# Optimization experiments

Measured on AMD Instinct MI355X. Metric: run time of the kernel, lower is better.

The kernel has to match this reference:

```python
import jax, jax.numpy as jnp
import numpy as np

N_CHARS = 256
EMB = 1024
HID = 2048
SEQ = 4096


def setup_inputs() -> dict:
    key = jax.random.key(0)
    ks = jax.random.split(key, 12)
    s = 0.02
    return {
        "input_seq": jax.random.randint(ks[0], (SEQ,), 0, N_CHARS),
        "hidden": jnp.zeros((HID,), jnp.float32),
        "cell": jnp.zeros((HID,), jnp.float32),
        "emb": jax.random.normal(ks[1], (N_CHARS, EMB), jnp.float32) * s,
        # gate weights stored as [concat, hidden] so step does z @ W + b
        "Wf": jax.random.normal(ks[2], (EMB + HID, HID), jnp.float32) * s,
        "bf": jnp.zeros((HID,), jnp.float32),
        "Wi": jax.random.normal(ks[3], (EMB + HID, HID), jnp.float32) * s,
        "bi": jnp.zeros((HID,), jnp.float32),
        "Wo": jax.random.normal(ks[4], (EMB + HID, HID), jnp.float32) * s,
        "bo": jnp.zeros((HID,), jnp.float32),
        "Wc": jax.random.normal(ks[5], (EMB + HID, HID), jnp.float32) * s,
        "bc": jnp.zeros((HID,), jnp.float32),
        "Wy": jax.random.normal(ks[6], (HID, N_CHARS), jnp.float32) * s,
        "by": jnp.zeros((N_CHARS,), jnp.float32),
    }


def reference(input_seq, hidden, cell, emb, Wf, bf, Wi, bi, Wo, bo, Wc, bc, Wy, by):
    x = emb[input_seq]  # [S, EMB] embedding lookup for whole sequence

    def step(carry, xt):
        h, c = carry
        z = jnp.concatenate([xt, h])           # [EMB+HID]
        f = jax.nn.sigmoid(z @ Wf + bf)        # forget gate
        i = jax.nn.sigmoid(z @ Wi + bi)        # input gate
        g = jnp.tanh(z @ Wc + bc)              # cell candidate
        o = jax.nn.sigmoid(z @ Wo + bo)        # output gate
        c_new = f * c + i * g
        h_new = o * jnp.tanh(c_new)
        y = h_new @ Wy + by                    # [N_CHARS]
        return (h_new, c_new), y

    (h_fin, c_fin), preds = jax.lax.scan(step, (hidden, cell), x)
    return preds, h_fin, c_fin
```

## Files before the change

### kernel.cpp

```cpp
#include <hip/hip_runtime.h>
#include <hip/hip_bf16.h>
#include <stdint.h>

#define NCH  256
#define EMB  1024
#define HID  2048
#define SEQL 4096

static constexpr size_t EG_OFF   = 0;
static constexpr size_t EG_BYTES = (size_t)NCH * 8192 * 4;
static constexpr size_t HS_OFF   = EG_OFF + EG_BYTES;
static constexpr size_t HS_BYTES = (size_t)SEQL * HID * 4;
static constexpr size_t HB_OFF   = HS_OFF + HS_BYTES;
static constexpr size_t HB_BYTES = 2 * HID * 8;
static constexpr size_t CF_OFF   = HB_OFF + HB_BYTES;
static constexpr size_t CF_BYTES = HID * 4;
static constexpr size_t WS_NEED  = CF_OFF + CF_BYTES;

__global__ __launch_bounds__(256) void eg_gemm(
    const float* __restrict__ emb,
    const float* __restrict__ Wf, const float* __restrict__ bf,
    const float* __restrict__ Wi, const float* __restrict__ bi,
    const float* __restrict__ Wo, const float* __restrict__ bo,
    const float* __restrict__ Wc, const float* __restrict__ bc,
    float* __restrict__ Eg)
{
    const int nb  = blockIdx.x & 63;
    const int cb  = blockIdx.x >> 6;
    const int tid = threadIdx.x;
    const int col = tid & 127;
    const int gate = col >> 5;
    const int jj   = col & 31;
    const int j    = nb * 32 + jj;
    const int mh   = tid >> 7;

    __shared__ float embT[32][65];
    __shared__ float Wt[32][128];

    float acc[32];
#pragma unroll
    for (int m = 0; m < 32; ++m) acc[m] = 0.f;

    for (int k0 = 0; k0 < EMB; k0 += 32) {
        __syncthreads();
        for (int i = tid; i < 64 * 32; i += 256) {
            int c = i >> 5, kk = i & 31;
            embT[kk][c] = emb[(size_t)(cb * 64 + c) * EMB + k0 + kk];
        }
        for (int i = tid; i < 32 * 128; i += 256) {
            int kk = i >> 7, cl = i & 127;
            int g2 = cl >> 5;
            int jx = nb * 32 + (cl & 31);
            const float* Wp = (g2 == 0) ? Wf : (g2 == 1) ? Wi : (g2 == 2) ? Wo : Wc;
            Wt[kk][cl] = Wp[(size_t)(k0 + kk) * HID + jx];
        }
        __syncthreads();
#pragma unroll 8
        for (int kk = 0; kk < 32; ++kk) {
            float w = Wt[kk][col];
#pragma unroll
            for (int m = 0; m < 32; ++m)
                acc[m] += embT[kk][mh * 32 + m] * w;
        }
    }
    const float* bias = (gate == 0) ? bf : (gate == 1) ? bi : (gate == 2) ? bo : bc;
    float bv = bias[j];
    for (int m = 0; m < 32; ++m) {
        int c = cb * 64 + mh * 32 + m;
        Eg[(size_t)c * 8192 + (j >> 3) * 32 + gate * 8 + (j & 7)] = acc[m] + bv;
    }
}

__device__ inline void bulk2(const void* p0, const void* p1, uint4& a, uint4& b)
{
    asm volatile(
        "global_load_dwordx4 %0, %2, off sc0 sc1\n\t"
        "global_load_dwordx4 %1, %3, off sc0 sc1\n\t"
        "s_waitcnt vmcnt(0)"
        : "=&v"(a), "=&v"(b)
        : "v"(p0), "v"(p1)
        : "memory");
}

#define REP32(M) M(0) M(1) M(2) M(3) M(4) M(5) M(6) M(7) M(8) M(9) M(10) M(11) \
  M(12) M(13) M(14) M(15) M(16) M(17) M(18) M(19) M(20) M(21) M(22) M(23)      \
  M(24) M(25) M(26) M(27) M(28) M(29) M(30) M(31)

__global__ __launch_bounds__(512, 2) void lstm_seq(
    const int*   __restrict__ seq,
    const float* __restrict__ h0,
    const float* __restrict__ c0,
    const float* __restrict__ Wf, const float* __restrict__ Wi,
    const float* __restrict__ Wo, const float* __restrict__ Wc,
    const float* __restrict__ Eg,
    float* __restrict__ Hs,
    unsigned long long* hb2, float* cfin)
{
    const int cu   = blockIdx.x;
    const int tid  = threadIdx.x;
    const int lane = tid & 63;
    const int wave = tid >> 6;
    const int g    = lane >> 4;
    const int kp   = lane & 15;
    const int jcol = cu * 8 + wave;

    const float* W = (g == 0) ? Wf : (g == 1) ? Wi : (g == 2) ? Wo : Wc;

    const float* Wb = W + (size_t)(1024 + kp * 4) * HID + jcol;
#define WDECL(i) float4 w##i;
    REP32(WDECL)
#undef WDECL
#define WLOAD(i) { w##i.x = Wb[(size_t)((i)*64+0)*HID]; \
                   w##i.y = Wb[(size_t)((i)*64+1)*HID]; \
                   w##i.z = Wb[(size_t)((i)*64+2)*HID]; \
                   w##i.w = Wb[(size_t)((i)*64+3)*HID]; }
    REP32(WLOAD)
#undef WLOAD

    __shared__ __align__(16) float h_lds[2][HID];
    __shared__ int seq_lds[SEQL];

    for (int i = tid; i < SEQL; i += 512) seq_lds[i] = seq[i];
    for (int i = tid; i < HID;  i += 512) h_lds[0][i] = h0[i];
    float c = c0[jcol];
    __syncthreads();

    for (int t = 0; t < SEQL; ++t) {
        float egv = Eg[(size_t)seq_lds[t] * 8192 + cu * 32 + g * 8 + wave];

        const float4* hp = (const float4*)(h_lds[t & 1]);
        float accv[4] = {0.f, 0.f, 0.f, 0.f};
#define WMAC(i) { float4 hv = hp[(i)*16 + kp]; \
                  accv[(i)&3] += w##i.x*hv.x + w##i.y*hv.y + w##i.z*hv.z + w##i.w*hv.w; }
        REP32(WMAC)
#undef WMAC
        float sum = (accv[0] + accv[1]) + (accv[2] + accv[3]);

        sum += __shfl_xor(sum, 1, 16);
        sum += __shfl_xor(sum, 2, 16);
        sum += __shfl_xor(sum, 4, 16);
        sum += __shfl_xor(sum, 8, 16);

        float pre = sum + egv;
        float act;
        if (g < 3) {
            act = 1.f / (1.f + __expf(-pre));
        } else {
            float e = __expf(2.f * pre);
            act = 1.f - 2.f / (e + 1.f);
        }
        float f_ = __shfl(act, 0,  64);
        float i_ = __shfl(act, 16, 64);
        float o_ = __shfl(act, 32, 64);
        float g_ = __shfl(act, 48, 64);

        c = f_ * c + i_ * g_;
        float e2 = __expf(2.f * c);
        float hn = o_ * (1.f - 2.f / (e2 + 1.f));

        if (lane == 0) {
            Hs[(size_t)t * HID + jcol] = hn;
            unsigned long long pk =
                ((unsigned long long)(unsigned)(t + 1) << 32) |
                (unsigned long long)__float_as_uint(hn);
            __hip_atomic_store(&hb2[(size_t)((t + 1) & 1) * HID + jcol], pk,
                               __ATOMIC_RELAXED, __HIP_MEMORY_SCOPE_AGENT);
        }

        if (t + 1 < SEQL) {
            const unsigned tgt = (unsigned)(t + 1);
            unsigned long long* sl = hb2 + (size_t)((t + 1) & 1) * HID;
            unsigned long long* mp = sl + 4 * tid;

            if ((unsigned)(__hip_atomic_load(mp, __ATOMIC_RELAXED,
                                             __HIP_MEMORY_SCOPE_AGENT) >> 32) < tgt) {
                do {
                    __builtin_amdgcn_s_sleep(1);
                } while ((unsigned)(__hip_atomic_load(mp, __ATOMIC_RELAXED,
                                                      __HIP_MEMORY_SCOPE_AGENT) >> 32) < tgt);
            }

            uint4 a, b;
            bulk2(mp, mp + 2, a, b);
            while (a.y < tgt || a.w < tgt || b.y < tgt || b.w < tgt) {
                __builtin_amdgcn_s_sleep(1);
                bulk2(mp, mp + 2, a, b);
            }

            float4 hv;
            hv.x = __uint_as_float(a.x);
            hv.y = __uint_as_float(a.z);
            hv.z = __uint_as_float(b.x);
            hv.w = __uint_as_float(b.z);
            ((float4*)h_lds[(t + 1) & 1])[tid] = hv;
            __syncthreads();
        }
    }

    if (lane == 0) cfin[jcol] = c;
}

__global__ __launch_bounds__(256) void y_gemm(
    const float* __restrict__ Hs, const float* __restrict__ Wy,
    const float* __restrict__ by, float* __restrict__ out)
{
    const int rb  = blockIdx.x * 16;
    const int tid = threadIdx.x;
    __shared__ float A[16][68];
    float acc[16];
#pragma unroll
    for (int r = 0; r < 16; ++r) acc[r] = 0.f;

    for (int k0 = 0; k0 < HID; k0 += 64) {
        __syncthreads();
        for (int i = tid; i < 16 * 64; i += 256) {
            int r = i >> 6, kk = i & 63;
            A[r][kk] = Hs[(size_t)(rb + r) * HID + k0 + kk];
        }
        __syncthreads();
#pragma unroll 8
        for (int kk = 0; kk < 64; ++kk) {
            float b = Wy[(size_t)(k0 + kk) * NCH + tid];
#pragma unroll
            for (int r = 0; r < 16; ++r) acc[r] += A[r][kk] * b;
        }
    }
    float bv = by[tid];
    for (int r = 0; r < 16; ++r)
        out[(size_t)(rb + r) * NCH + tid] = acc[r] + bv;
}

__global__ void fin_copy(const float* __restrict__ Hs,
                         const float* __restrict__ cfin,
                         float* __restrict__ out)
{
    int i = blockIdx.x * 256 + threadIdx.x;
    if (i < HID)
        out[(size_t)SEQL * NCH + i] = Hs[(size_t)(SEQL - 1) * HID + i];
    else
        out[(size_t)SEQL * NCH + i] = cfin[i - HID];
}

extern "C" void kernel_launch(void* const* d_in, const int* in_sizes, int n_in,
                              void* d_out, int out_size, void* d_ws, size_t ws_size,
                              hipStream_t stream)
{
    if (n_in < 14 || ws_size < WS_NEED) return;

    const int*   seq = (const int*)  d_in[0];
    const float* h0  = (const float*)d_in[1];
    const float* c0  = (const float*)d_in[2];
    const float* emb = (const float*)d_in[3];
    const float* Wf  = (const float*)d_in[4];
    const float* bf  = (const float*)d_in[5];
    const float* Wi  = (const float*)d_in[6];
    const float* bi  = (const float*)d_in[7];
    const float* Wo  = (const float*)d_in[8];
    const float* bo  = (const float*)d_in[9];
    const float* Wc  = (const float*)d_in[10];
    const float* bc  = (const float*)d_in[11];
    const float* Wy  = (const float*)d_in[12];
    const float* by  = (const float*)d_in[13];

    char* ws = (char*)d_ws;
    float*              Eg   = (float*)(ws + EG_OFF);
    float*              Hs   = (float*)(ws + HS_OFF);
    unsigned long long* hb2  = (unsigned long long*)(ws + HB_OFF);
    float*              cfin = (float*)(ws + CF_OFF);
    float*              out  = (float*)d_out;

    hipMemsetAsync(hb2, 0, HB_BYTES, stream);

    eg_gemm<<<256, 256, 0, stream>>>(emb, Wf, bf, Wi, bi, Wo, bo, Wc, bc, Eg);

    lstm_seq<<<256, 512, 0, stream>>>(seq, h0, c0, Wf, Wi, Wo, Wc, Eg,
                                      Hs, hb2, cfin);

    y_gemm<<<256, 256, 0, stream>>>(Hs, Wy, by, out);

    fin_copy<<<16, 256, 0, stream>>>(Hs, cfin, out);
}
```

Baseline: 25.69 ms.

## Poll published hidden state from a single wave instead of all waves

```diff
diff --git a/kernel.cpp b/kernel.cpp
--- a/kernel.cpp
+++ b/kernel.cpp
@@ -71,20 +71,12 @@
     }
 }
 
-__device__ inline void bulk2(const void* p0, const void* p1, uint4& a, uint4& b)
-{
-    asm volatile(
-        "global_load_dwordx4 %0, %2, off sc0 sc1\n\t"
-        "global_load_dwordx4 %1, %3, off sc0 sc1\n\t"
-        "s_waitcnt vmcnt(0)"
-        : "=&v"(a), "=&v"(b)
-        : "v"(p0), "v"(p1)
-        : "memory");
-}
-
 #define REP32(M) M(0) M(1) M(2) M(3) M(4) M(5) M(6) M(7) M(8) M(9) M(10) M(11) \
   M(12) M(13) M(14) M(15) M(16) M(17) M(18) M(19) M(20) M(21) M(22) M(23)      \
   M(24) M(25) M(26) M(27) M(28) M(29) M(30) M(31)
+
+#define REP16(M) M(0) M(1) M(2) M(3) M(4) M(5) M(6) M(7) M(8) M(9) M(10) M(11) \
+  M(12) M(13) M(14) M(15)
 
 __global__ __launch_bounds__(512, 2) void lstm_seq(
     const int*   __restrict__ seq,
@@ -158,41 +150,64 @@
         float e2 = __expf(2.f * c);
         float hn = o_ * (1.f - 2.f / (e2 + 1.f));
 
+        const unsigned tgt  = (unsigned)(t + 1);
+        const unsigned bsel = (unsigned)((t + 1) & 1);
+
         if (lane == 0) {
             Hs[(size_t)t * HID + jcol] = hn;
             unsigned long long pk =
-                ((unsigned long long)(unsigned)(t + 1) << 32) |
+                ((unsigned long long)tgt << 32) |
                 (unsigned long long)__float_as_uint(hn);
-            __hip_atomic_store(&hb2[(size_t)((t + 1) & 1) * HID + jcol], pk,
-                               __ATOMIC_RELAXED, __HIP_MEMORY_SCOPE_AGENT);
+            (void)__hip_atomic_exchange(&hb2[(size_t)bsel * HID + jcol], pk,
+                                        __ATOMIC_RELAXED,
+                                        __HIP_MEMORY_SCOPE_AGENT);
         }
 
         if (t + 1 < SEQL) {
-            const unsigned tgt = (unsigned)(t + 1);
-            unsigned long long* sl = hb2 + (size_t)((t + 1) & 1) * HID;
-            unsigned long long* mp = sl + 4 * tid;
-
-            if ((unsigned)(__hip_atomic_load(mp, __ATOMIC_RELAXED,
-                                             __HIP_MEMORY_SCOPE_AGENT) >> 32) < tgt) {
-                do {
+            if (wave == 0) {
+                const unsigned long long* bp =
+                    hb2 + (size_t)bsel * HID + (size_t)lane * 32;
+#define VDECL(q) uint4 v##q;
+                REP16(VDECL)
+#undef VDECL
+                for (;;) {
+                    asm volatile(
+                        "global_load_dwordx4 %0,  %16, off sc0 sc1\n\t"
+                        "global_load_dwordx4 %1,  %16, off offset:16 sc0 sc1\n\t"
+                        "global_load_dwordx4 %2,  %16, off offset:32 sc0 sc1\n\t"
+                        "global_load_dwordx4 %3,  %16, off offset:48 sc0 sc1\n\t"
+                        "global_load_dwordx4 %4,  %16, off offset:64 sc0 sc1\n\t"
+                        "global_load_dwordx4 %5,  %16, off offset:80 sc0 sc1\n\t"
+                        "global_load_dwordx4 %6,  %16, off offset:96 sc0 sc1\n\t"
+                        "global_load_dwordx4 %7,  %16, off offset:112 sc0 sc1\n\t"
+                        "global_load_dwordx4 %8,  %16, off offset:128 sc0 sc1\n\t"
+                        "global_load_dwordx4 %9,  %16, off offset:144 sc0 sc1\n\t"
+                        "global_load_dwordx4 %10, %16, off offset:160 sc0 sc1\n\t"
+                        "global_load_dwordx4 %11, %16, off offset:176 sc0 sc1\n\t"
+                        "global_load_dwordx4 %12, %16, off offset:192 sc0 sc1\n\t"
+                        "global_load_dwordx4 %13, %16, off offset:208 sc0 sc1\n\t"
+                        "global_load_dwordx4 %14, %16, off offset:224 sc0 sc1\n\t"
+                        "global_load_dwordx4 %15, %16, off offset:240 sc0 sc1\n\t"
+                        "s_waitcnt vmcnt(0)"
+                        : "=&v"(v0), "=&v"(v1), "=&v"(v2), "=&v"(v3),
+                          "=&v"(v4), "=&v"(v5), "=&v"(v6), "=&v"(v7),
+                          "=&v"(v8), "=&v"(v9), "=&v"(v10), "=&v"(v11),
+                          "=&v"(v12), "=&v"(v13), "=&v"(v14), "=&v"(v15)
+                        : "v"(bp)
+                        : "memory");
+                    unsigned m = v0.y;
+#define MM(q) m = (v##q.y < m) ? v##q.y : m; m = (v##q.w < m) ? v##q.w : m;
+                    REP16(MM)
+#undef MM
+                    if (m >= tgt) break;
                     __builtin_amdgcn_s_sleep(1);
-                } while ((unsigned)(__hip_atomic_load(mp, __ATOMIC_RELAXED,
-                                                      __HIP_MEMORY_SCOPE_AGENT) >> 32) < tgt);
+                }
+                float2* dst = (float2*)(h_lds[bsel]) + lane * 16;
+#define ST(q) dst[q] = make_float2(__uint_as_float(v##q.x), \
+                                   __uint_as_float(v##q.z));
+                REP16(ST)
+#undef ST
             }
-
-            uint4 a, b;
-            bulk2(mp, mp + 2, a, b);
-            while (a.y < tgt || a.w < tgt || b.y < tgt || b.w < tgt) {
-                __builtin_amdgcn_s_sleep(1);
-                bulk2(mp, mp + 2, a, b);
-            }
-
-            float4 hv;
-            hv.x = __uint_as_float(a.x);
-            hv.y = __uint_as_float(a.z);
-            hv.z = __uint_as_float(b.x);
-            hv.w = __uint_as_float(b.z);
-            ((float4*)h_lds[(t + 1) & 1])[tid] = hv;
             __syncthreads();
         }
     }
```

After: 40.94 ms. +59.3%, slower.

## Replicate hidden-state broadcast buffer into 8 copies to spread polling traffic

Applied to the files above, without the earlier changes.

```diff
diff --git a/kernel.cpp b/kernel.cpp
--- a/kernel.cpp
+++ b/kernel.cpp
@@ -12,7 +12,7 @@
 static constexpr size_t HS_OFF   = EG_OFF + EG_BYTES;
 static constexpr size_t HS_BYTES = (size_t)SEQL * HID * 4;
 static constexpr size_t HB_OFF   = HS_OFF + HS_BYTES;
-static constexpr size_t HB_BYTES = 2 * HID * 8;
+static constexpr size_t HB_BYTES = (size_t)8 * 2 * HID * 8;
 static constexpr size_t CF_OFF   = HB_OFF + HB_BYTES;
 static constexpr size_t CF_BYTES = HID * 4;
 static constexpr size_t WS_NEED  = CF_OFF + CF_BYTES;
@@ -69,17 +69,6 @@
         int c = cb * 64 + mh * 32 + m;
         Eg[(size_t)c * 8192 + (j >> 3) * 32 + gate * 8 + (j & 7)] = acc[m] + bv;
     }
-}
-
-__device__ inline void bulk2(const void* p0, const void* p1, uint4& a, uint4& b)
-{
-    asm volatile(
-        "global_load_dwordx4 %0, %2, off sc0 sc1\n\t"
-        "global_load_dwordx4 %1, %3, off sc0 sc1\n\t"
-        "s_waitcnt vmcnt(0)"
-        : "=&v"(a), "=&v"(b)
-        : "v"(p0), "v"(p1)
-        : "memory");
 }
 
 #define REP32(M) M(0) M(1) M(2) M(3) M(4) M(5) M(6) M(7) M(8) M(9) M(10) M(11) \
@@ -103,6 +92,7 @@
     const int g    = lane >> 4;
     const int kp   = lane & 15;
     const int jcol = cu * 8 + wave;
+    const int grp  = cu & 7;
 
     const float* W = (g == 0) ? Wf : (g == 1) ? Wi : (g == 2) ? Wo : Wc;
 
@@ -158,41 +148,43 @@
         float e2 = __expf(2.f * c);
         float hn = o_ * (1.f - 2.f / (e2 + 1.f));
 
-        if (lane == 0) {
+        const unsigned tgt  = (unsigned)(t + 1);
+        const unsigned bsel = (unsigned)((t + 1) & 1);
+
+        {
+            unsigned long long pk =
+                ((unsigned long long)tgt << 32) |
+                (unsigned long long)__float_as_uint(hn);
+            if (lane < 8)
+                __hip_atomic_store(
+                    &hb2[((size_t)lane * 2 + bsel) * HID + jcol], pk,
+                    __ATOMIC_RELAXED, __HIP_MEMORY_SCOPE_AGENT);
+        }
+        if (lane == 0)
             Hs[(size_t)t * HID + jcol] = hn;
-            unsigned long long pk =
-                ((unsigned long long)(unsigned)(t + 1) << 32) |
-                (unsigned long long)__float_as_uint(hn);
-            __hip_atomic_store(&hb2[(size_t)((t + 1) & 1) * HID + jcol], pk,
-                               __ATOMIC_RELAXED, __HIP_MEMORY_SCOPE_AGENT);
-        }
 
         if (t + 1 < SEQL) {
-            const unsigned tgt = (unsigned)(t + 1);
-            unsigned long long* sl = hb2 + (size_t)((t + 1) & 1) * HID;
-            unsigned long long* mp = sl + 4 * tid;
-
-            if ((unsigned)(__hip_atomic_load(mp, __ATOMIC_RELAXED,
-                                             __HIP_MEMORY_SCOPE_AGENT) >> 32) < tgt) {
-                do {
-                    __builtin_amdgcn_s_sleep(1);
-                } while ((unsigned)(__hip_atomic_load(mp, __ATOMIC_RELAXED,
-                                                      __HIP_MEMORY_SCOPE_AGENT) >> 32) < tgt);
-            }
-
-            uint4 a, b;
-            bulk2(mp, mp + 2, a, b);
-            while (a.y < tgt || a.w < tgt || b.y < tgt || b.w < tgt) {
-                __builtin_amdgcn_s_sleep(1);
-                bulk2(mp, mp + 2, a, b);
-            }
+            const unsigned long long* mp =
+                hb2 + ((size_t)grp * 2 + bsel) * HID + 4 * (size_t)tid;
+            unsigned long long x0, x1, x2, x3;
+            do {
+                x0 = __hip_atomic_load(mp + 0, __ATOMIC_RELAXED,
+                                       __HIP_MEMORY_SCOPE_AGENT);
+                x1 = __hip_atomic_load(mp + 1, __ATOMIC_RELAXED,
+                                       __HIP_MEMORY_SCOPE_AGENT);
+                x2 = __hip_atomic_load(mp + 2, __ATOMIC_RELAXED,
+                                       __HIP_MEMORY_SCOPE_AGENT);
+                x3 = __hip_atomic_load(mp + 3, __ATOMIC_RELAXED,
+                                       __HIP_MEMORY_SCOPE_AGENT);
+            } while ((unsigned)(x0 >> 32) < tgt || (unsigned)(x1 >> 32) < tgt ||
+                     (unsigned)(x2 >> 32) < tgt || (unsigned)(x3 >> 32) < tgt);
 
             float4 hv;
-            hv.x = __uint_as_float(a.x);
-            hv.y = __uint_as_float(a.z);
-            hv.z = __uint_as_float(b.x);
-            hv.w = __uint_as_float(b.z);
-            ((float4*)h_lds[(t + 1) & 1])[tid] = hv;
+            hv.x = __uint_as_float((unsigned)x0);
+            hv.y = __uint_as_float((unsigned)x1);
+            hv.z = __uint_as_float((unsigned)x2);
+            hv.w = __uint_as_float((unsigned)x3);
+            ((float4*)h_lds[bsel])[tid] = hv;
             __syncthreads();
         }
     }
```

Result: slower. 26.96 ms (+4.9%).
